# Kernel tuning notes

Measured on AMD Instinct MI355X. Metric: run time of the kernel, lower is better.

Reference implementation:

```python
import math
import jax, jax.numpy as jnp
import numpy as np


def conv2d(x, w, stride=1, padding=0, groups=1):
    return jax.lax.conv_general_dilated(
        x, w, (stride, stride), [(padding, padding), (padding, padding)],
        feature_group_count=groups, dimension_numbers=('NCHW', 'OIHW', 'NCHW'))


def bn_relu(x, g, b, eps=1e-5):
    # training-mode batchnorm (batch statistics, biased var) + ReLU
    m = x.mean(axis=(0, 2, 3), keepdims=True)
    v = x.var(axis=(0, 2, 3), keepdims=True)
    y = (x - m) * jax.lax.rsqrt(v + eps)
    return jax.nn.relu(y * g[None, :, None, None] + b[None, :, None, None])


def up2x(x):
    B, C, H, W = x.shape
    return jax.image.resize(x, (B, C, 2 * H, 2 * W), 'bilinear')


def pos2d(C, H, W):
    # faithful port of ReasonDecoder.pos2d -> [H*W, 1, C]
    dm = C // 2
    div = jnp.exp(jnp.arange(0.0, dm, 2.0) * (-(math.log(10000.0) / dm)))  # [dm//2]
    pos_w = jnp.arange(0.0, W)[:, None]
    pos_h = jnp.arange(0.0, H)[:, None]
    sw = jnp.sin(pos_w * div).T  # [dm//2, W]
    cw = jnp.cos(pos_w * div).T
    sh = jnp.sin(pos_h * div).T  # [dm//2, H]
    ch = jnp.cos(pos_h * div).T
    pe = jnp.zeros((C, H, W))
    pe = pe.at[0:dm:2].set(jnp.broadcast_to(sw[:, None, :], (dm // 2, H, W)))
    pe = pe.at[1:dm:2].set(jnp.broadcast_to(cw[:, None, :], (dm // 2, H, W)))
    pe = pe.at[dm::2].set(jnp.broadcast_to(sh[:, :, None], (dm // 2, H, W)))
    pe = pe.at[dm + 1::2].set(jnp.broadcast_to(ch[:, :, None], (dm // 2, H, W)))
    return pe.reshape(C, 1, H * W).transpose(2, 1, 0)


def setup_inputs() -> dict:
    key = jax.random.key(0)
    ks = jax.random.split(key, 32)
    B, C, H, W = 8, 512, 32, 32
    Cv = 256  # in_dim of Projector
    KS = 3
    s = 0.02
    inp = {
        'image_embeddings': jax.random.normal(ks[0], (B, C, H, W), jnp.float32),
        'sparse_prompt_embeddings': jax.random.normal(ks[1], (B, 2, C), jnp.float32),
        'state': jax.random.normal(ks[2], (B, C), jnp.float32),
        'multimask_output': 0,
        # stand-in transformer: single linear on (src + pos)
        'W_t': jax.random.normal(ks[3], (C, C), jnp.float32) * s,
        'iou_token': jax.random.normal(ks[4], (1, C), jnp.float32) * s,
        'mask_tokens': jax.random.normal(ks[5], (4, C), jnp.float32) * s,
        # Projector.vis
        'vis_conv1_w': jax.random.normal(ks[6], (2 * Cv, 2 * Cv, 3, 3), jnp.float32) * s,
        'vis_bn1_g': jnp.ones((2 * Cv,), jnp.float32),
        'vis_bn1_b': jnp.zeros((2 * Cv,), jnp.float32),
        'vis_conv2_w': jax.random.normal(ks[7], (Cv, 2 * Cv, 3, 3), jnp.float32) * s,
        'vis_bn2_g': jnp.ones((Cv,), jnp.float32),
        'vis_bn2_b': jnp.zeros((Cv,), jnp.float32),
        'vis_conv3_w': jax.random.normal(ks[8], (Cv, Cv, 1, 1), jnp.float32) * s,
        'vis_conv3_b': jnp.zeros((Cv,), jnp.float32),
        # Projector.txt -> Linear(512, 256*3*3 + 1)
        'txt_w': jax.random.normal(ks[9], (Cv * KS * KS + 1, C), jnp.float32) * s,
        'txt_b': jnp.zeros((Cv * KS * KS + 1,), jnp.float32),
        # 1x1 convs as linears
        'ln_ans_w': jax.random.normal(ks[10], (512, 512), jnp.float32) * s,
        'ln_ans_b': jnp.zeros((512,), jnp.float32),
        'ln_ans2_w': jax.random.normal(ks[11], (128, 512), jnp.float32) * s,
        'ln_ans2_b': jnp.zeros((128,), jnp.float32),
        # router: Linear(1024,256) -> ReLU -> Linear(256,8)
        'router_w1': jax.random.normal(ks[12], (256, 1024), jnp.float32) * s,
        'router_b1': jnp.zeros((256,), jnp.float32),
        'router_w2': jax.random.normal(ks[13], (8, 256), jnp.float32) * s,
        'router_b2': jnp.zeros((8,), jnp.float32),
        # 8 experts: Linear(128, 23) each, stacked
        'experts_w': jax.random.normal(ks[14], (8, 23, 128), jnp.float32) * s,
        'experts_b': jnp.zeros((8, 23), jnp.float32),
    }
    return inp


def reference(image_embeddings, sparse_prompt_embeddings, state, multimask_output,
              W_t, iou_token, mask_tokens,
              vis_conv1_w, vis_bn1_g, vis_bn1_b,
              vis_conv2_w, vis_bn2_g, vis_bn2_b,
              vis_conv3_w, vis_conv3_b,
              txt_w, txt_b, ln_ans_w, ln_ans_b, ln_ans2_w, ln_ans2_b,
              router_w1, router_b1, router_w2, router_b2,
              experts_w, experts_b):
    B, C, H, W = image_embeddings.shape
    pe = pos2d(C, H, W)  # [HW,1,C]

    # tokens = [iou, mask tokens, sparse prompts] (passed to transformer; hs unused)
    out_tok = jnp.concatenate([iou_token, mask_tokens], axis=0)  # [5,C]
    tokens = jnp.concatenate(
        [jnp.broadcast_to(out_tok[None], (B,) + out_tok.shape), sparse_prompt_embeddings], axis=1)
    del tokens  # hs is discarded by predict_masks

    # stand-in transformer: src_out = Linear(src_flat + pos)
    src_flat = image_embeddings.reshape(B, C, H * W).transpose(0, 2, 1) + pe[:, 0, :][None]  # [B,HW,C]
    src_flat = jnp.einsum('bnc,dc->bnd', src_flat, W_t)
    src = src_flat.transpose(0, 2, 1).reshape(B, C, H, W)

    # ---- Projector ----
    ans = src.mean(axis=(2, 3))                              # global avg pool [B,512]
    ans_vec = ans @ ln_ans_w.T + ln_ans_b                    # 1x1 conv [B,512]

    x = up2x(src)
    x = bn_relu(conv2d(x, vis_conv1_w, padding=1), vis_bn1_g, vis_bn1_b)
    x = up2x(x)
    x = bn_relu(conv2d(x, vis_conv2_w, padding=1), vis_bn2_g, vis_bn2_b)
    x = conv2d(x, vis_conv3_w) + vis_conv3_b[None, :, None, None]  # [B,256,4H,4W]
    Bx, Cx, Hx, Wx = x.shape

    qa = jnp.concatenate([state, ans_vec], axis=1)           # [B,1024]
    o = jax.nn.softmax(qa, axis=1) * qa
    half = o.shape[1] // 2
    word = o[:, :half] + o[:, half:]                         # [B,512]
    word = word @ txt_w.T + txt_b                            # [B, 256*9+1]
    dyn_w = word[:, :-1].reshape(B, Cx, 3, 3)                # per-sample conv weights
    dyn_b = word[:, -1]                                      # [B]

    xg = x.reshape(1, B * Cx, Hx, Wx)
    out = conv2d(xg, dyn_w, padding=1, groups=B) + dyn_b[None, :, None, None]  # [1,B,Hx,Wx]
    masks = out.transpose(1, 0, 2, 3)                        # [B,1,Hx,Wx]

    gates = jax.nn.softmax(
        jax.nn.relu(qa @ router_w1.T + router_b1) @ router_w2.T + router_b2, axis=1)  # [B,8]
    feat128 = ans_vec @ ln_ans2_w.T + ln_ans2_b              # [B,128]
    logits = jnp.einsum('be,eof,bf->bo', gates, experts_w, feat128) + gates @ experts_b  # [B,23]

    masks = masks[:, 1:, :, :] if multimask_output else masks[:, 0:1, :, :]
    return masks, logits, src
```

## Files before the change

### kernel.cpp

```cpp
#include <hip/hip_runtime.h>
#include <hip/hip_bf16.h>

typedef __attribute__((ext_vector_type(8))) short short8;
typedef __attribute__((ext_vector_type(4))) short shortx4;
typedef __attribute__((ext_vector_type(4))) float floatx4;
typedef __attribute__((ext_vector_type(16))) float floatx16;

#define F2BF __float2bfloat16
#define BF2F __bfloat162float

#define WS_W4R2   0UL
#define WS_WRO2   9437184UL
#define WS_WRO1   11796480UL
#define WS_Y1     16515072UL
#define WS_Y2     50069504UL
#define WS_W4R1   50069504UL
#define WS_A      68943872UL
#define WS_WTB    77332480UL
#define WS_SRCB   77856768UL
#define WS_STATS  117178368UL
#define WS_ANS    117186560UL
#define WS_QA     117207040UL
#define WS_ANSV   117239808UL
#define WS_WORD   117256192UL
#define WS_WORD2  117272576UL
#define WS_EFFW   117346336UL
#define WS_EFFB   117420064UL
#define WS_HID    117420352UL

#define OUT_LOGITS 131072
#define OUT_SRC    131256

__device__ __forceinline__ float inp(const void* p, long i, int isbf) {
    return isbf ? BF2F(((const __hip_bfloat16*)p)[i]) : ((const float*)p)[i];
}
__device__ __forceinline__ void outw(void* p, long i, float v, int isbf) {
    if (isbf) ((__hip_bfloat16*)p)[i] = F2BF(v);
    else      ((float*)p)[i] = v;
}
__device__ __forceinline__ float bfbits2f(short s) {
    unsigned int u = ((unsigned int)(unsigned short)s) << 16;
    float f; __builtin_memcpy(&f, &u, 4); return f;
}
__device__ __forceinline__ short f2bfbits(float f) {
    __hip_bfloat16 h = F2BF(f);
    short s; __builtin_memcpy(&s, &h, 2); return s;
}

__device__ __forceinline__ int detect_bf(const void* img) {
    const unsigned short* u = (const unsigned short*)img;
    int l = threadIdx.x & 63;
    int c = 0;
#pragma unroll
    for (int k = 0; k < 8; ++k) {
        int e = (u[(l * 8 + k) * 2] >> 7) & 0xFF;
        c += (e >= 100 && e <= 150) ? 1 : 0;
    }
    for (int off = 32; off; off >>= 1) c += __shfl_xor(c, off, 64);
    return c > 307;
}

__device__ __forceinline__ float pe_val(int n, int c) {
    float pos = (c < 256) ? (float)(n & 31) : (float)(n >> 5);
    int i = ((c < 256) ? c : (c - 256)) >> 1;
    float ang = pos * expf(-0.0719557841560639f * (float)i);
    return (c & 1) ? cosf(ang) : sinf(ang);
}

__global__ void k_pre(const void* __restrict__ img, const void* __restrict__ cw1,
                      const void* __restrict__ cw2, const void* __restrict__ Wt,
                      __hip_bfloat16* __restrict__ A,
                      __hip_bfloat16* __restrict__ W4R1, __hip_bfloat16* __restrict__ W4R2,
                      __hip_bfloat16* __restrict__ WRo1, __hip_bfloat16* __restrict__ WRo2,
                      __hip_bfloat16* __restrict__ WTB) {
    int isbf = detect_bf(img);
    int bid = blockIdx.x, tid = threadIdx.x;
    __shared__ float LS[2304];
    if (bid < 4096) {
        int nt = bid & 31, ct = (bid >> 5) & 15, b = bid >> 9;
        int tx = tid & 31, ty = tid >> 5;
        int c0 = ct * 32, n0 = nt * 32;
        for (int j = 0; j < 4; ++j) {
            int c = c0 + ty + j * 8;
            LS[(ty + j * 8) * 33 + tx] = inp(img, ((long)(b * 512 + c)) * 1024 + n0 + tx, isbf);
        }
        __syncthreads();
        for (int j = 0; j < 4; ++j) {
            int n = n0 + ty + j * 8, c = c0 + tx;
            A[((long)(b * 1024 + n)) * 512 + c] = F2BF(LS[tx * 33 + ty + j * 8] + pe_val(n, c));
        }
    } else if (bid < 5632) {
        int bb = bid - 4096;
        const void* w; __hip_bfloat16 *w4, *wo; int Cout, r0;
        if (bb < 1024) { w = cw1; w4 = W4R1; wo = WRo1; Cout = 512; r0 = bb * 256; }
        else           { w = cw2; w4 = W4R2; wo = WRo2; Cout = 256; r0 = (bb - 1024) * 256; }
        int Cout4 = Cout << 2;
        int co = r0 >> 9, ci0 = r0 & 511;
        for (int e = tid; e < 2304; e += 256) LS[e] = inp(w, (long)r0 * 9 + e, isbf);
        __syncthreads();
        int ci = ci0 + tid;
        int cc = ci >> 5, cw = ci & 31;
        float w9[9];
#pragma unroll
        for (int t = 0; t < 9; ++t) w9[t] = LS[tid * 9 + t];
#pragma unroll
        for (int t = 0; t < 9; ++t)
            wo[((long)(t * 16 + cc) * Cout + co) * 32 + cw] = F2BF(w9[t]);
        const float BY[2][3][3] = {{{0.75f, 0.25f, 0.f}, {0.25f, 0.75f, 0.75f}, {0.f, 0.f, 0.25f}},
                                   {{0.25f, 0.f, 0.f},  {0.75f, 0.75f, 0.25f}, {0.f, 0.25f, 0.75f}}};
#pragma unroll
        for (int p = 0; p < 4; ++p) {
            int py = p >> 1, px = p & 1;
#pragma unroll
            for (int dy = 0; dy < 3; ++dy)
#pragma unroll
            for (int dx = 0; dx < 3; ++dx) {
                float v = 0.f;
#pragma unroll
                for (int ky = 0; ky < 3; ++ky)
#pragma unroll
                for (int kx = 0; kx < 3; ++kx)
                    v += BY[py][dy][ky] * BY[px][dx][kx] * w9[ky * 3 + kx];
                w4[((long)((dy * 3 + dx) * 16 + cc) * Cout4 + p * Cout + co) * 32 + cw] = F2BF(v);
            }
        }
    } else {
        for (int i = (bid - 5632) * 256 + tid; i < 512 * 512; i += 256 * 256)
            WTB[i] = F2BF(inp(Wt, i, isbf));
    }
}

__global__ __launch_bounds__(256) void k_gemm1(const __hip_bfloat16* __restrict__ A,
                                               const __hip_bfloat16* __restrict__ Bw,
                                               __hip_bfloat16* __restrict__ srcB,
                                               void* __restrict__ dst,
                                               float* __restrict__ ANS,
                                               const void* __restrict__ img) {
    int isbf = detect_bf(img);
    __shared__ __align__(16) __hip_bfloat16 As[128 * 32];
    __shared__ __align__(16) __hip_bfloat16 Bs[128 * 32];
    int m0 = blockIdx.x * 128, n0 = blockIdx.y * 128;
    int tid = threadIdx.x;
    int wave = tid >> 6, l = tid & 63, lm = l & 15, q = l >> 4;
    int wm = wave & 1, wn = wave >> 1;
    int m_0 = tid >> 2, qq0 = tid & 3;
    int m_1 = (tid + 256) >> 2, qq1 = qq0;
    const __hip_bfloat16* aA0 = A + ((long)(m0 + m_0)) * 512 + qq0 * 8;
    const __hip_bfloat16* aB0 = Bw + ((long)(n0 + m_0)) * 512 + qq0 * 8;
    const __hip_bfloat16* aA1 = A + ((long)(m0 + m_1)) * 512 + qq1 * 8;
    const __hip_bfloat16* aB1 = Bw + ((long)(n0 + m_1)) * 512 + qq1 * 8;
    int wA0 = m_0 * 32 + qq0 * 8, wA1 = m_1 * 32 + qq1 * 8;
    short8 rA0 = *(const short8*)(aA0), rB0 = *(const short8*)(aB0);
    short8 rA1 = *(const short8*)(aA1), rB1 = *(const short8*)(aB1);
    floatx4 zero4 = {0.f, 0.f, 0.f, 0.f};
    floatx4 acc[4][4];
    for (int i = 0; i < 4; ++i) for (int j = 0; j < 4; ++j) acc[i][j] = zero4;
    for (int k0 = 0; k0 < 512; k0 += 32) {
        __syncthreads();
        *(short8*)(As + wA0) = rA0; *(short8*)(Bs + wA0) = rB0;
        *(short8*)(As + wA1) = rA1; *(short8*)(Bs + wA1) = rB1;
        __syncthreads();
        if (k0 < 480) {
            rA0 = *(const short8*)(aA0 + k0 + 32); rB0 = *(const short8*)(aB0 + k0 + 32);
            rA1 = *(const short8*)(aA1 + k0 + 32); rB1 = *(const short8*)(aB1 + k0 + 32);
        }
        short8 af[4], bfv[4];
#pragma unroll
        for (int t = 0; t < 4; ++t) af[t] = *(short8*)(As + (wm * 64 + t * 16 + lm) * 32 + q * 8);
#pragma unroll
        for (int t = 0; t < 4; ++t) bfv[t] = *(short8*)(Bs + (wn * 64 + t * 16 + lm) * 32 + q * 8);
#pragma unroll
        for (int i = 0; i < 4; ++i)
#pragma unroll
            for (int j = 0; j < 4; ++j)
                acc[i][j] = __builtin_amdgcn_mfma_f32_16x16x32_bf16(af[i], bfv[j], acc[i][j], 0, 0, 0);
    }
    int b = m0 >> 10, hw0 = m0 & 1023;
    float cs[4] = {0.f, 0.f, 0.f, 0.f};
#pragma unroll
    for (int i = 0; i < 4; ++i)
#pragma unroll
        for (int j = 0; j < 4; ++j) {
            int mrow = wm * 64 + i * 16 + q * 4;
            int n = n0 + wn * 64 + j * 16 + lm;
            long mg = (long)(m0 + mrow);
#pragma unroll
            for (int r = 0; r < 4; ++r) {
                float v = acc[i][j][r];
                srcB[(mg + r) * 512 + n] = F2BF(v);
                cs[j] += v;
            }
            long obase = (long)OUT_SRC + ((long)(b * 512 + n)) * 1024 + hw0 + mrow;
            if (isbf) {
                shortx4 pk = { f2bfbits(acc[i][j][0]), f2bfbits(acc[i][j][1]),
                               f2bfbits(acc[i][j][2]), f2bfbits(acc[i][j][3]) };
                *(shortx4*)((__hip_bfloat16*)dst + obase) = pk;
            } else {
                floatx4 pk = { acc[i][j][0], acc[i][j][1], acc[i][j][2], acc[i][j][3] };
                *(floatx4*)((float*)dst + obase) = pk;
            }
        }
#pragma unroll
    for (int j = 0; j < 4; ++j) {
        cs[j] += __shfl_xor(cs[j], 16);
        cs[j] += __shfl_xor(cs[j], 32);
    }
    __syncthreads();
    float* CS = (float*)Bs;
    if (wm == 1 && q == 0) {
#pragma unroll
        for (int j = 0; j < 4; ++j) CS[wn * 64 + j * 16 + lm] = cs[j];
    }
    __syncthreads();
    if (wm == 0 && q == 0) {
#pragma unroll
        for (int j = 0; j < 4; ++j) {
            int n = n0 + wn * 64 + j * 16 + lm;
            atomicAdd(ANS + b * 512 + n, cs[j] + CS[wn * 64 + j * 16 + lm]);
        }
    }
}

__global__ void k_ansvec(const float* __restrict__ ANS, const void* __restrict__ lw,
                         const void* __restrict__ lb, float* __restrict__ ansv,
                         const void* __restrict__ img) {
    int isbf = detect_bf(img);
    int b = blockIdx.x, dt = blockIdx.y, tid = threadIdx.x;
    __shared__ float aL[512];
    __shared__ float R[256];
    aL[tid] = ANS[b * 512 + tid] * (1.f / 1024.f);
    aL[tid + 256] = ANS[b * 512 + tid + 256] * (1.f / 1024.f);
    __syncthreads();
    int d = dt * 64 + (tid >> 2), cl = tid & 3;
    float acc = 0.f;
    for (int k = 0; k < 128; ++k) {
        int c = cl + 4 * k;
        acc += aL[c] * inp(lw, (long)d * 512 + c, isbf);
    }
    R[tid] = acc;
    __syncthreads();
    if (cl == 0)
        ansv[b * 512 + d] = R[tid] + R[tid + 1] + R[tid + 2] + R[tid + 3] + inp(lb, d, isbf);
}

__global__ void k_word(const float* __restrict__ ansv, const void* __restrict__ state,
                       float* __restrict__ qa, float* __restrict__ word,
                       const void* __restrict__ img) {
    int isbf = detect_bf(img);
    int b = blockIdx.x, tid = threadIdx.x;
    __shared__ float L[1024];
    __shared__ float red[256];
    L[tid] = inp(state, b * 512 + tid, isbf);
    L[tid + 256] = inp(state, b * 512 + tid + 256, isbf);
    L[tid + 512] = ansv[b * 512 + tid];
    L[tid + 768] = ansv[b * 512 + tid + 256];
    __syncthreads();
    for (int j = tid; j < 1024; j += 256) qa[b * 1024 + j] = L[j];
    float m = fmaxf(fmaxf(L[tid], L[tid + 256]), fmaxf(L[tid + 512], L[tid + 768]));
    red[tid] = m; __syncthreads();
    for (int s = 128; s > 0; s >>= 1) { if (tid < s) red[tid] = fmaxf(red[tid], red[tid + s]); __syncthreads(); }
    float M = red[0]; __syncthreads();
    float z = expf(L[tid] - M) + expf(L[tid + 256] - M) + expf(L[tid + 512] - M) + expf(L[tid + 768] - M);
    red[tid] = z; __syncthreads();
    for (int s = 128; s > 0; s >>= 1) { if (tid < s) red[tid] += red[tid + s]; __syncthreads(); }
    float Z = red[0];
    for (int j = tid; j < 512; j += 256) {
        float o1 = expf(L[j] - M) / Z * L[j];
        float o2 = expf(L[j + 512] - M) / Z * L[j + 512];
        word[b * 512 + j] = o1 + o2;
    }
}

__global__ void k_txt(const float* __restrict__ word, const void* __restrict__ tw,
                      const void* __restrict__ tb, float* __restrict__ word2,
                      const void* __restrict__ img) {
    int isbf = detect_bf(img);
    int n = blockIdx.x, tid = threadIdx.x;
    __shared__ float wL[8][512];
    __shared__ float red[256 * 8];
    for (int e = tid; e < 4096; e += 256) wL[e >> 9][e & 511] = word[e];
    __syncthreads();
    float acc[8] = {0, 0, 0, 0, 0, 0, 0, 0};
    for (int c = tid; c < 512; c += 256) {
        float tv = inp(tw, (long)n * 512 + c, isbf);
        for (int b = 0; b < 8; ++b) acc[b] += wL[b][c] * tv;
    }
    for (int b = 0; b < 8; ++b) red[tid * 8 + b] = acc[b];
    __syncthreads();
    for (int s = 128; s > 0; s >>= 1) {
        if (tid < s) for (int b = 0; b < 8; ++b) red[tid * 8 + b] += red[(tid + s) * 8 + b];
        __syncthreads();
    }
    if (tid < 8) word2[tid * 2305 + n] = red[tid] + inp(tb, n, isbf);
}

__global__ void k_eff(const float* __restrict__ word2, const void* __restrict__ w3,
                      const void* __restrict__ b3, float* __restrict__ effw,
                      float* __restrict__ effb, const void* __restrict__ img) {
    int isbf = detect_bf(img);
    int bid = blockIdx.x;
    int b = bid / 9, tap = bid - b * 9;
    int tid = threadIdx.x;
    __shared__ float dw[256];
    dw[tid] = word2[b * 2305 + tid * 9 + tap];
    __syncthreads();
    float acc = 0.f;
    for (int c = 0; c < 256; ++c) acc += dw[c] * inp(w3, c * 256 + tid, isbf);
    effw[(b * 9 + tap) * 256 + tid] = acc;
    if (tid == 0) {
        float e = 0.f;
        for (int c = 0; c < 256; ++c) e += dw[c] * inp(b3, c, isbf);
        effb[b * 9 + tap] = e;
    }
}

__device__ __forceinline__ void epi32(const floatx16& Acc, int pxbase, int co4,
        int csh, int Cout, int tY, int tX, int b, int OW2, int hi,
        __hip_bfloat16* __restrict__ out, float& s1, float& s2) {
    int par = co4 >> csh; int co = co4 & (Cout - 1);
    int fyo = par >> 1, fxo = par & 1;
#pragma unroll
    for (int r = 0; r < 16; ++r) {
        int row = (r & 3) + 8 * (r >> 2) + 4 * hi;
        int px = pxbase + row;
        int fy = (((tY << 3) + (px >> 4)) << 1) + fyo;
        int fx = (((tX << 4) + (px & 15)) << 1) + fxo;
        float v = Acc[r];
        out[(((long)(b * OW2 + fy)) * OW2 + fx) * Cout + co] = F2BF(v);
        s1 += v; s2 += v * v;
    }
}

__global__ __launch_bounds__(256, 3) void k_conv4(const __hip_bfloat16* __restrict__ in,
        const __hip_bfloat16* __restrict__ w4, __hip_bfloat16* __restrict__ out,
        int inH, int inW, int Cout, float* __restrict__ s1o, float* __restrict__ s2o,
        const float* __restrict__ bnS1, const float* __restrict__ bnS2,
        const void* __restrict__ g, const void* __restrict__ bb, float invN,
        const void* __restrict__ img) {
    int Cout4 = Cout << 2;
    int csh = (Cout == 512) ? 9 : 8;
    int tXn = inW >> 4, tYn = inH >> 3;
    int bid = blockIdx.y;
    int tX = bid % tXn; int tmp = bid / tXn; int tY = tmp % tYn; int b = tmp / tYn;
    int co0 = blockIdx.x * 128;
    __shared__ __align__(16) __hip_bfloat16 Hs[180 * 40];
    __shared__ float scT[512], shT[512];
    int tid = threadIdx.x;
    int l = tid & 63, l31 = l & 31, hi = l >> 5;
    int wave = tid >> 6;
    int wm = wave & 1, wn = wave >> 1;
    int dobn = (bnS1 != nullptr);
    if (dobn) {
        int isbf = detect_bf(img);
        for (int c = tid; c < 512; c += 256) {
            float m = bnS1[c] * invN, var = bnS2[c] * invN - m * m;
            float sc = inp(g, c, isbf) * rsqrtf(var + 1e-5f);
            scT[c] = sc; shT[c] = inp(bb, c, isbf) - m * sc;
        }
    }
    int R0 = (tY << 3) - 1, C0 = (tX << 4) - 1;
    long base = (long)b * inH * inW;
    int sub = tid & 3;
    const __hip_bfloat16* ga[3];
    int wo[3];
#pragma unroll
    for (int s = 0; s < 3; ++s) {
        int gi = tid + s * 256;
        int p = gi >> 2; if (p > 179) p = 179;
        int hy = p / 18, hx = p - hy * 18;
        int gr = R0 + hy; gr = gr < 0 ? 0 : (gr > inH - 1 ? inH - 1 : gr);
        int gc = C0 + hx; gc = gc < 0 ? 0 : (gc > inW - 1 ? inW - 1 : gc);
        ga[s] = in + (base + (long)gr * inW + gc) * 512 + sub * 8;
        wo[s] = p * 40 + sub * 8;
    }
    int has2 = (tid < 208);
    short8 r0 = *(const short8*)(ga[0]);
    short8 r1 = *(const short8*)(ga[1]);
    short8 r2 = {0, 0, 0, 0, 0, 0, 0, 0};
    if (has2) r2 = *(const short8*)(ga[2]);
    int hb0, hb1;
    {
        int px0 = wm * 64 + l31;
        int px1 = px0 + 32;
        hb0 = ((px0 >> 4) * 18 + (px0 & 15)) * 40 + hi * 8;
        hb1 = ((px1 >> 4) * 18 + (px1 & 15)) * 40 + hi * 8;
    }
    const __hip_bfloat16* wl = w4 + ((long)(co0 + wn * 64 + l31)) * 32 + hi * 8;
    long TS = (long)Cout4 * 512;
    long CS = (long)Cout4 * 32;
    short8 wS0[4], wS1[4], wS2[4];
#define LDW(S, t, c) { const __hip_bfloat16* _p = wl + (long)(t) * TS + (long)(c) * CS; \
    S[0] = *(const short8*)(_p);            S[1] = *(const short8*)(_p + 16); \
    S[2] = *(const short8*)(_p + 1024);     S[3] = *(const short8*)(_p + 1024 + 16); }
    floatx16 zero16 = {0,0,0,0,0,0,0,0,0,0,0,0,0,0,0,0};
    floatx16 a00 = zero16, a01 = zero16, a10 = zero16, a11 = zero16;
    LDW(wS0, 0, 0);
    for (int ci0 = 0; ci0 < 512; ci0 += 32) {
        int cc = ci0 >> 5;
        __syncthreads();
        if (dobn) {
            float scv[8], shv[8];
#pragma unroll
            for (int k = 0; k < 8; ++k) { int c = ci0 + sub * 8 + k; scv[k] = scT[c]; shv[k] = shT[c]; }
#pragma unroll
            for (int k = 0; k < 8; ++k) {
                float f0 = bfbits2f(r0[k]) * scv[k] + shv[k]; r0[k] = f2bfbits(f0 > 0.f ? f0 : 0.f);
                float f1 = bfbits2f(r1[k]) * scv[k] + shv[k]; r1[k] = f2bfbits(f1 > 0.f ? f1 : 0.f);
                float f2 = bfbits2f(r2[k]) * scv[k] + shv[k]; r2[k] = f2bfbits(f2 > 0.f ? f2 : 0.f);
            }
        }
        *(short8*)(Hs + wo[0]) = r0;
        *(short8*)(Hs + wo[1]) = r1;
        if (has2) *(short8*)(Hs + wo[2]) = r2;
        __syncthreads();
        if (ci0 < 480) {
            r0 = *(const short8*)(ga[0] + ci0 + 32);
            r1 = *(const short8*)(ga[1] + ci0 + 32);
            if (has2) r2 = *(const short8*)(ga[2] + ci0 + 32);
        }
#pragma unroll
        for (int tap = 0; tap < 9; ++tap) {
            {
                int nt = tap + 1, ncc = cc;
                if (nt == 9) { nt = 0; ncc = cc + 1; }
                if (ncc < 16) {
                    if (((tap + 1) % 3) == 0)      { LDW(wS0, nt, ncc); }
                    else if (((tap + 1) % 3) == 1) { LDW(wS1, nt, ncc); }
                    else                            { LDW(wS2, nt, ncc); }
                }
            }
            int dy = tap / 3, dx = tap - dy * 3;
            int ho = (dy * 18 + dx) * 40;
            short8 af00 = *(const short8*)(Hs + hb0 + ho);
            short8 af01 = *(const short8*)(Hs + hb0 + ho + 16);
            short8 af10 = *(const short8*)(Hs + hb1 + ho);
            short8 af11 = *(const short8*)(Hs + hb1 + ho + 16);
            if ((tap % 3) == 0) {
                a00 = __builtin_amdgcn_mfma_f32_32x32x16_bf16(af00, wS0[0], a00, 0, 0, 0);
                a00 = __builtin_amdgcn_mfma_f32_32x32x16_bf16(af01, wS0[1], a00, 0, 0, 0);
                a01 = __builtin_amdgcn_mfma_f32_32x32x16_bf16(af00, wS0[2], a01, 0, 0, 0);
                a01 = __builtin_amdgcn_mfma_f32_32x32x16_bf16(af01, wS0[3], a01, 0, 0, 0);
                a10 = __builtin_amdgcn_mfma_f32_32x32x16_bf16(af10, wS0[0], a10, 0, 0, 0);
                a10 = __builtin_amdgcn_mfma_f32_32x32x16_bf16(af11, wS0[1], a10, 0, 0, 0);
                a11 = __builtin_amdgcn_mfma_f32_32x32x16_bf16(af10, wS0[2], a11, 0, 0, 0);
                a11 = __builtin_amdgcn_mfma_f32_32x32x16_bf16(af11, wS0[3], a11, 0, 0, 0);
            } else if ((tap % 3) == 1) {
                a00 = __builtin_amdgcn_mfma_f32_32x32x16_bf16(af00, wS1[0], a00, 0, 0, 0);
                a00 = __builtin_amdgcn_mfma_f32_32x32x16_bf16(af01, wS1[1], a00, 0, 0, 0);
                a01 = __builtin_amdgcn_mfma_f32_32x32x16_bf16(af00, wS1[2], a01, 0, 0, 0);
                a01 = __builtin_amdgcn_mfma_f32_32x32x16_bf16(af01, wS1[3], a01, 0, 0, 0);
                a10 = __builtin_amdgcn_mfma_f32_32x32x16_bf16(af10, wS1[0], a10, 0, 0, 0);
                a10 = __builtin_amdgcn_mfma_f32_32x32x16_bf16(af11, wS1[1], a10, 0, 0, 0);
                a11 = __builtin_amdgcn_mfma_f32_32x32x16_bf16(af10, wS1[2], a11, 0, 0, 0);
                a11 = __builtin_amdgcn_mfma_f32_32x32x16_bf16(af11, wS1[3], a11, 0, 0, 0);
            } else {
                a00 = __builtin_amdgcn_mfma_f32_32x32x16_bf16(af00, wS2[0], a00, 0, 0, 0);
                a00 = __builtin_amdgcn_mfma_f32_32x32x16_bf16(af01, wS2[1], a00, 0, 0, 0);
                a01 = __builtin_amdgcn_mfma_f32_32x32x16_bf16(af00, wS2[2], a01, 0, 0, 0);
                a01 = __builtin_amdgcn_mfma_f32_32x32x16_bf16(af01, wS2[3], a01, 0, 0, 0);
                a10 = __builtin_amdgcn_mfma_f32_32x32x16_bf16(af10, wS2[0], a10, 0, 0, 0);
                a10 = __builtin_amdgcn_mfma_f32_32x32x16_bf16(af11, wS2[1], a10, 0, 0, 0);
                a11 = __builtin_amdgcn_mfma_f32_32x32x16_bf16(af10, wS2[2], a11, 0, 0, 0);
                a11 = __builtin_amdgcn_mfma_f32_32x32x16_bf16(af11, wS2[3], a11, 0, 0, 0);
            }
        }
    }
#undef LDW
    int OW2 = inW << 1;
    float s1v0 = 0.f, s2v0 = 0.f, s1v1 = 0.f, s2v1 = 0.f;
    {
        int pxb0 = wm * 64, pxb1 = wm * 64 + 32;
        int co4a = co0 + wn * 64 + l31;
        int co4b = co4a + 32;
        epi32(a00, pxb0, co4a, csh, Cout, tY, tX, b, OW2, hi, out, s1v0, s2v0);
        epi32(a10, pxb1, co4a, csh, Cout, tY, tX, b, OW2, hi, out, s1v0, s2v0);
        epi32(a01, pxb0, co4b, csh, Cout, tY, tX, b, OW2, hi, out, s1v1, s2v1);
        epi32(a11, pxb1, co4b, csh, Cout, tY, tX, b, OW2, hi, out, s1v1, s2v1);
    }
    s1v0 += __shfl_xor(s1v0, 32); s2v0 += __shfl_xor(s2v0, 32);
    s1v1 += __shfl_xor(s1v1, 32); s2v1 += __shfl_xor(s2v1, 32);
    __syncthreads();
    float* RB = (float*)Hs;
    if (wm == 1 && hi == 0) {
        int i0 = wn * 64 + l31, i1 = i0 + 32;
        RB[i0] = s1v0; RB[128 + i0] = s2v0;
        RB[i1] = s1v1; RB[128 + i1] = s2v1;
    }
    __syncthreads();
    if (wm == 0 && hi == 0) {
        int i0 = wn * 64 + l31, i1 = i0 + 32;
        atomicAdd(s1o + ((co0 + i0) & (Cout - 1)), s1v0 + RB[i0]);
        atomicAdd(s2o + ((co0 + i0) & (Cout - 1)), s2v0 + RB[128 + i0]);
        atomicAdd(s1o + ((co0 + i1) & (Cout - 1)), s1v1 + RB[i1]);
        atomicAdd(s2o + ((co0 + i1) & (Cout - 1)), s2v1 + RB[128 + i1]);
    }
}

__global__ __launch_bounds__(256) void k_efix(const __hip_bfloat16* __restrict__ in,
        __hip_bfloat16* __restrict__ Y, const __hip_bfloat16* __restrict__ wRo,
        int inW, int Cout, int ebase,
        float* __restrict__ s1o, float* __restrict__ s2o) {
    int OW = inW << 1;
    int coT = Cout >> 6;
    int b = blockIdx.x / coT, cot = blockIdx.x - b * coT;
    int co0 = cot << 6;
    int e = ebase + blockIdx.y;
    __shared__ __align__(16) __hip_bfloat16 E[130 * 40];
    __shared__ __align__(16) __hip_bfloat16 Lline[64 * 32];
    int tid = threadIdx.x;
    int wave = tid >> 6, l = tid & 63, lm = l & 15, q = l >> 4;
    int mspan = OW >> 2;
    int ilim = OW >> 6;
    int mb = wave * mspan;
    floatx4 zero4 = {0.f, 0.f, 0.f, 0.f};
    floatx4 acc[2][4];
    for (int i = 0; i < 2; ++i) for (int j = 0; j < 4; ++j) acc[i][j] = zero4;
    int lineG = inW * 4;
    int eG = (OW + 2) * 4;
    int haveL = (tid < lineG);
    const __hip_bfloat16* lbase = in;
    {
        int x = tid >> 2, sb = tid & 3;
        long gidx;
        if (e < 2) { int R = (e == 0) ? 0 : inW - 1; gidx = (long)(b * inW + R) * inW + x; }
        else       { int Cc = (e == 2) ? 0 : inW - 1; gidx = (long)(b * inW + x) * inW + Cc; }
        if (x >= inW) gidx = (long)b * inW * inW;
        lbase = in + gidx * 512 + sb * 8;
    }
    short8 rl = {0, 0, 0, 0, 0, 0, 0, 0};
    if (haveL) rl = *(const short8*)(lbase);
    for (int ci0 = 0; ci0 < 512; ci0 += 32) {
        __syncthreads();
        if (haveL) *(short8*)(Lline + tid * 8) = rl;
        __syncthreads();
        if (ci0 < 480 && haveL) rl = *(const short8*)(lbase + ci0 + 32);
        for (int t = tid; t < eG; t += 256) {
            int f1 = t >> 2, sb = t & 3;
            int f = f1 - 1;
            short8 res = {0, 0, 0, 0, 0, 0, 0, 0};
            if (f < 0 || f >= OW) {
                if (e < 2) { int xx = (f < 0) ? 0 : inW - 1; res = *(const short8*)(Lline + (xx * 4 + sb) * 8); }
            } else {
                int x0; float w0;
                if (f & 1) { x0 = f >> 1; w0 = 0.75f; } else { x0 = (f >> 1) - 1; w0 = 0.25f; }
                int x1 = x0 + 1;
                if (x0 < 0) x0 = 0;
                if (x1 > inW - 1) x1 = inW - 1;
                short8 v0 = *(const short8*)(Lline + (x0 * 4 + sb) * 8);
                short8 v1 = *(const short8*)(Lline + (x1 * 4 + sb) * 8);
                float w1c = 1.f - w0;
#pragma unroll
                for (int k = 0; k < 8; ++k)
                    res[k] = f2bfbits(w0 * bfbits2f(v0[k]) + w1c * bfbits2f(v1[k]));
            }
            *(short8*)(E + f1 * 40 + sb * 8) = res;
        }
        __syncthreads();
        int cc = ci0 >> 5;
#pragma unroll
        for (int t = 0; t < 3; ++t) {
            int tap = (e == 0) ? t : (e == 1) ? (6 + t) : (e == 2) ? (t * 3) : (t * 3 + 2);
            short8 bfv[4];
#pragma unroll
            for (int j = 0; j < 4; ++j)
                bfv[j] = *(const short8*)(wRo + ((long)(tap * 16 + cc) * Cout + co0 + j * 16 + lm) * 32 + q * 8);
#pragma unroll
            for (int i = 0; i < 2; ++i) {
                if (i < ilim) {
                    short8 af = *(const short8*)(E + (mb + i * 16 + lm + t) * 40 + q * 8);
#pragma unroll
                    for (int j = 0; j < 4; ++j)
                        acc[i][j] = __builtin_amdgcn_mfma_f32_16x16x32_bf16(af, bfv[j], acc[i][j], 0, 0, 0);
                }
            }
        }
    }
    float d1s[4] = {0.f, 0.f, 0.f, 0.f}, d2s[4] = {0.f, 0.f, 0.f, 0.f};
    for (int i = 0; i < ilim; ++i)
#pragma unroll
    for (int j = 0; j < 4; ++j) {
        int co = co0 + j * 16 + lm;
#pragma unroll
        for (int r = 0; r < 4; ++r) {
            int m = mb + i * 16 + q * 4 + r;
            int fy, fx;
            if (e == 0) { fy = 0; fx = m; }
            else if (e == 1) { fy = OW - 1; fx = m; }
            else if (e == 2) { fy = m; fx = 0; }
            else { fy = m; fx = OW - 1; }
            long a = (((long)(b * OW + fy)) * OW + fx) * Cout + co;
            float vo = BF2F(Y[a]);
            float vn = vo - acc[i][j][r];
            Y[a] = F2BF(vn);
            d1s[j] += vn - vo;
            d2s[j] += vn * vn - vo * vo;
        }
    }
#pragma unroll
    for (int j = 0; j < 4; ++j) {
        d1s[j] += __shfl_xor(d1s[j], 16); d1s[j] += __shfl_xor(d1s[j], 32);
        d2s[j] += __shfl_xor(d2s[j], 16); d2s[j] += __shfl_xor(d2s[j], 32);
    }
    if (q == 0) {
#pragma unroll
        for (int j = 0; j < 4; ++j) {
            atomicAdd(s1o + co0 + j * 16 + lm, d1s[j]);
            atomicAdd(s2o + co0 + j * 16 + lm, d2s[j]);
        }
    }
}

__global__ __launch_bounds__(256) void k_masks(const __hip_bfloat16* __restrict__ x2,
                                               const float* __restrict__ effw,
                                               const float* __restrict__ effb,
                                               const float* __restrict__ word2,
                                               void* __restrict__ mout,
                                               const float* __restrict__ s1,
                                               const float* __restrict__ s2,
                                               const void* __restrict__ g,
                                               const void* __restrict__ bb, float invN,
                                               const void* __restrict__ img) {
    int isbf = detect_bf(img);
    int bid = blockIdx.x;
    int tX = bid & 15, tY = (bid >> 4) & 15, b = bid >> 8;
    __shared__ __align__(16) __hip_bfloat16 H[100 * 264];
    __shared__ __align__(16) float EW[9 * 256];
    __shared__ float EB[9];
    __shared__ float sc2T[256];
    __shared__ float sh2T[256];
    int tid = threadIdx.x;
    {
        float m = s1[tid] * invN, var = s2[tid] * invN - m * m;
        float sc = inp(g, tid, isbf) * rsqrtf(var + 1e-5f);
        sc2T[tid] = sc; sh2T[tid] = inp(bb, tid, isbf) - m * sc;
    }
    __syncthreads();
    for (int e = tid; e < 3200; e += 256) {
        int c8 = e & 31, p = e >> 5;
        int hy = p / 10, hx = p - hy * 10;
        int gy = tY * 8 + hy - 1, gx = tX * 8 + hx - 1;
        short8 res = {0, 0, 0, 0, 0, 0, 0, 0};
        if (gy >= 0 && gy < 128 && gx >= 0 && gx < 128) {
            short8 raw = *(const short8*)(x2 + (((long)(b * 128 + gy)) * 128 + gx) * 256 + c8 * 8);
#pragma unroll
            for (int k = 0; k < 8; ++k) {
                int c = c8 * 8 + k;
                float v = bfbits2f(raw[k]) * sc2T[c] + sh2T[c];
                res[k] = f2bfbits(v > 0.f ? v : 0.f);
            }
        }
        *(short8*)(H + p * 264 + c8 * 8) = res;
    }
    for (int e = tid; e < 2304; e += 256) EW[e] = effw[b * 2304 + e];
    if (tid < 9) EB[tid] = effb[b * 9 + tid];
    __syncthreads();
    int px = tid & 63, part = tid >> 6;
    int py = px >> 3, pxc = px & 7;
    int cbase = part * 64;
    float acc = 0.f;
    for (int tap = 0; tap < 9; ++tap) {
        int ky = tap / 3, kx = tap - ky * 3;
        int hp = (py + ky) * 10 + pxc + kx;
        const __hip_bfloat16* hrow = H + (long)hp * 264 + cbase;
        const float* erow = EW + tap * 256 + cbase;
#pragma unroll
        for (int c8 = 0; c8 < 8; ++c8) {
            short8 h8 = *(const short8*)(hrow + c8 * 8);
            floatx4 e0 = *(const floatx4*)(erow + c8 * 8);
            floatx4 e1 = *(const floatx4*)(erow + c8 * 8 + 4);
            acc += bfbits2f(h8[0]) * e0[0] + bfbits2f(h8[1]) * e0[1] +
                   bfbits2f(h8[2]) * e0[2] + bfbits2f(h8[3]) * e0[3] +
                   bfbits2f(h8[4]) * e1[0] + bfbits2f(h8[5]) * e1[1] +
                   bfbits2f(h8[6]) * e1[2] + bfbits2f(h8[7]) * e1[3];
        }
    }
    float (*red)[64] = (float(*)[64])sc2T;
    red[part][px] = acc;
    __syncthreads();
    if (part == 0) {
        float s = red[0][px] + red[1][px] + red[2][px] + red[3][px];
        int oy = tY * 8 + py, ox = tX * 8 + pxc;
        float bias = word2[b * 2305 + 2304];
        for (int tap = 0; tap < 9; ++tap) {
            int ky = tap / 3, kx = tap - ky * 3;
            int iy = oy + ky - 1, ix = ox + kx - 1;
            if (iy >= 0 && iy < 128 && ix >= 0 && ix < 128) bias += EB[tap];
        }
        outw(mout, b * 16384 + oy * 128 + ox, s + bias, isbf);
    }
}

__global__ void k_hid(const float* __restrict__ qa, const void* __restrict__ w1,
                      const void* __restrict__ b1, float* __restrict__ hid,
                      const void* __restrict__ img) {
    int isbf = detect_bf(img);
    int b = blockIdx.x, ht = blockIdx.y, tid = threadIdx.x;
    __shared__ float qL[1024];
    __shared__ float R[256];
    for (int j = tid; j < 1024; j += 256) qL[j] = qa[b * 1024 + j];
    __syncthreads();
    int h = ht * 64 + (tid >> 2), cl = tid & 3;
    float acc = 0.f;
    for (int k = 0; k < 256; ++k) {
        int c = cl + 4 * k;
        acc += qL[c] * inp(w1, (long)h * 1024 + c, isbf);
    }
    R[tid] = acc;
    __syncthreads();
    if (cl == 0) {
        float v = R[tid] + R[tid + 1] + R[tid + 2] + R[tid + 3] + inp(b1, h, isbf);
        hid[b * 256 + h] = v > 0.f ? v : 0.f;
    }
}

__global__ void k_logits(const float* __restrict__ hid, const float* __restrict__ ansv,
                         const void* __restrict__ w2, const void* __restrict__ b2,
                         const void* __restrict__ lw2, const void* __restrict__ lb2,
                         const void* __restrict__ ew, const void* __restrict__ ebias,
                         void* __restrict__ out, const void* __restrict__ img) {
    int isbf = detect_bf(img);
    int b = blockIdx.x, tid = threadIdx.x;
    __shared__ float hidL[256], avL[512], gates[8], feat[128], R[256];
    hidL[tid] = hid[b * 256 + tid];
    for (int j = tid; j < 512; j += 256) avL[j] = ansv[b * 512 + j];
    __syncthreads();
    if (tid < 8) {
        float gl = inp(b2, tid, isbf);
        for (int j = 0; j < 256; ++j) gl += hidL[j] * inp(w2, tid * 256 + j, isbf);
        gates[tid] = gl;
    }
    int f = tid >> 1, half = tid & 1;
    float acc = 0.f;
    for (int k = 0; k < 256; ++k) {
        int c = half + 2 * k;
        acc += avL[c] * inp(lw2, (long)f * 512 + c, isbf);
    }
    R[tid] = acc;
    __syncthreads();
    if (tid == 0) {
        float mx = gates[0];
        for (int e = 1; e < 8; ++e) mx = fmaxf(mx, gates[e]);
        float z = 0.f;
        for (int e = 0; e < 8; ++e) { gates[e] = expf(gates[e] - mx); z += gates[e]; }
        for (int e = 0; e < 8; ++e) gates[e] /= z;
    }
    if (half == 0) feat[f] = R[tid] + R[tid + 1] + inp(lb2, f, isbf);
    __syncthreads();
    if (tid < 23) {
        float a = 0.f;
        for (int e = 0; e < 8; ++e) {
            float d = inp(ebias, e * 23 + tid, isbf);
            for (int ff = 0; ff < 128; ++ff) d += inp(ew, (e * 23 + tid) * 128 + ff, isbf) * feat[ff];
            a += gates[e] * d;
        }
        outw(out, OUT_LOGITS + b * 23 + tid, a, isbf);
    }
}

extern "C" void kernel_launch(void* const* d_in, const int* in_sizes, int n_in,
                              void* d_out, int out_size, void* d_ws, size_t ws_size,
                              hipStream_t stream) {
    (void)in_sizes; (void)n_in; (void)out_size; (void)ws_size;
    const void* img   = d_in[0];
    const void* state = d_in[2];
    const void* Wt    = d_in[4];
    const void* cw1   = d_in[7];
    const void* g1    = d_in[8];
    const void* bb1   = d_in[9];
    const void* cw2   = d_in[10];
    const void* g2    = d_in[11];
    const void* bb2   = d_in[12];
    const void* w3    = d_in[13];
    const void* b3    = d_in[14];
    const void* txtw  = d_in[15];
    const void* txtb  = d_in[16];
    const void* lnw   = d_in[17];
    const void* lnb   = d_in[18];
    const void* lnw2  = d_in[19];
    const void* lnb2  = d_in[20];
    const void* rw1   = d_in[21];
    const void* rb1   = d_in[22];
    const void* rw2   = d_in[23];
    const void* rb2   = d_in[24];
    const void* ew    = d_in[25];
    const void* eb    = d_in[26];

    char* ws = (char*)d_ws;
    __hip_bfloat16* W4R2 = (__hip_bfloat16*)(ws + WS_W4R2);
    __hip_bfloat16* WRO2 = (__hip_bfloat16*)(ws + WS_WRO2);
    __hip_bfloat16* WRO1 = (__hip_bfloat16*)(ws + WS_WRO1);
    __hip_bfloat16* Y1   = (__hip_bfloat16*)(ws + WS_Y1);
    __hip_bfloat16* Y2   = (__hip_bfloat16*)(ws + WS_Y2);
    __hip_bfloat16* W4R1 = (__hip_bfloat16*)(ws + WS_W4R1);
    __hip_bfloat16* A    = (__hip_bfloat16*)(ws + WS_A);
    __hip_bfloat16* WTB  = (__hip_bfloat16*)(ws + WS_WTB);
    __hip_bfloat16* SRCB = (__hip_bfloat16*)(ws + WS_SRCB);
    float* S1A = (float*)(ws + WS_STATS);
    float* S2A = S1A + 512;
    float* S1B = S1A + 1024;
    float* S2B = S1A + 1536;
    float* ANS   = (float*)(ws + WS_ANS);
    float* QA    = (float*)(ws + WS_QA);
    float* ANSV  = (float*)(ws + WS_ANSV);
    float* WORD  = (float*)(ws + WS_WORD);
    float* WORD2 = (float*)(ws + WS_WORD2);
    float* EFFW  = (float*)(ws + WS_EFFW);
    float* EFFB  = (float*)(ws + WS_EFFB);
    float* HID   = (float*)(ws + WS_HID);

    hipMemsetAsync(ws + WS_STATS, 0, 24576, stream);

    k_pre<<<5888, 256, 0, stream>>>(img, cw1, cw2, Wt, A, W4R1, W4R2, WRO1, WRO2, WTB);
    k_gemm1<<<dim3(64, 4), 256, 0, stream>>>(A, WTB, SRCB, d_out, ANS, img);
    k_ansvec<<<dim3(8, 8), 256, 0, stream>>>(ANS, lnw, lnb, ANSV, img);
    k_word<<<8, 256, 0, stream>>>(ANSV, state, QA, WORD, img);
    k_txt<<<2305, 256, 0, stream>>>(WORD, txtw, txtb, WORD2, img);
    k_eff<<<72, 256, 0, stream>>>(WORD2, w3, b3, EFFW, EFFB, img);
    k_conv4<<<dim3(16, 64), 256, 0, stream>>>(SRCB, W4R1, Y1, 32, 32, 512, S1A, S2A,
                                              nullptr, nullptr, nullptr, nullptr, 0.f, img);
    k_efix<<<dim3(64, 2), 256, 0, stream>>>(SRCB, Y1, WRO1, 32, 512, 0, S1A, S2A);
    k_efix<<<dim3(64, 2), 256, 0, stream>>>(SRCB, Y1, WRO1, 32, 512, 2, S1A, S2A);
    k_conv4<<<dim3(8, 256), 256, 0, stream>>>(Y1, W4R2, Y2, 64, 64, 256, S1B, S2B,
                                              S1A, S2A, g1, bb1, 1.f / 32768.f, img);
    k_efix<<<dim3(32, 2), 256, 0, stream>>>(Y1, Y2, WRO2, 64, 256, 0, S1B, S2B);
    k_efix<<<dim3(32, 2), 256, 0, stream>>>(Y1, Y2, WRO2, 64, 256, 2, S1B, S2B);
    k_masks<<<2048, 256, 0, stream>>>(Y2, EFFW, EFFB, WORD2, d_out,
                                      S1B, S2B, g2, bb2, 1.f / 131072.f, img);
    k_hid<<<dim3(8, 4), 256, 0, stream>>>(QA, rw1, rb1, HID, img);
    k_logits<<<8, 256, 0, stream>>>(HID, ANSV, rw2, rb2, lnw2, lnb2, ew, eb, d_out, img);
}
```

Before: 1.094 ms.

## Double-buffer conv4 halo tile in LDS with one barrier per channel chunk

```diff
diff --git a/kernel.cpp b/kernel.cpp
--- a/kernel.cpp
+++ b/kernel.cpp
@@ -343,21 +343,13 @@
     int bid = blockIdx.y;
     int tX = bid % tXn; int tmp = bid / tXn; int tY = tmp % tYn; int b = tmp / tYn;
     int co0 = blockIdx.x * 128;
-    __shared__ __align__(16) __hip_bfloat16 Hs[180 * 40];
+    __shared__ __align__(16) __hip_bfloat16 Hs[2][180 * 40];
     __shared__ float scT[512], shT[512];
     int tid = threadIdx.x;
     int l = tid & 63, l31 = l & 31, hi = l >> 5;
     int wave = tid >> 6;
     int wm = wave & 1, wn = wave >> 1;
     int dobn = (bnS1 != nullptr);
-    if (dobn) {
-        int isbf = detect_bf(img);
-        for (int c = tid; c < 512; c += 256) {
-            float m = bnS1[c] * invN, var = bnS2[c] * invN - m * m;
-            float sc = inp(g, c, isbf) * rsqrtf(var + 1e-5f);
-            scT[c] = sc; shT[c] = inp(bb, c, isbf) - m * sc;
-        }
-    }
     int R0 = (tY << 3) - 1, C0 = (tX << 4) - 1;
     long base = (long)b * inH * inW;
     int sub = tid & 3;
@@ -378,6 +370,31 @@
     short8 r1 = *(const short8*)(ga[1]);
     short8 r2 = {0, 0, 0, 0, 0, 0, 0, 0};
     if (has2) r2 = *(const short8*)(ga[2]);
+    if (dobn) {
+        int isbf = detect_bf(img);
+        for (int c = tid; c < 512; c += 256) {
+            float m = bnS1[c] * invN, var = bnS2[c] * invN - m * m;
+            float sc = inp(g, c, isbf) * rsqrtf(var + 1e-5f);
+            scT[c] = sc; shT[c] = inp(bb, c, isbf) - m * sc;
+        }
+    }
+    __syncthreads();
+    if (dobn) {
+        int cb = sub * 8;
+#pragma unroll
+        for (int k = 0; k < 8; ++k) {
+            float sc = scT[cb + k], sh = shT[cb + k];
+            float f0 = bfbits2f(r0[k]) * sc + sh; r0[k] = f2bfbits(f0 > 0.f ? f0 : 0.f);
+            float f1 = bfbits2f(r1[k]) * sc + sh; r1[k] = f2bfbits(f1 > 0.f ? f1 : 0.f);
+            float f2 = bfbits2f(r2[k]) * sc + sh; r2[k] = f2bfbits(f2 > 0.f ? f2 : 0.f);
+        }
+    }
+    *(short8*)(Hs[0] + wo[0]) = r0;
+    *(short8*)(Hs[0] + wo[1]) = r1;
+    if (has2) *(short8*)(Hs[0] + wo[2]) = r2;
+    r0 = *(const short8*)(ga[0] + 32);
+    r1 = *(const short8*)(ga[1] + 32);
+    if (has2) r2 = *(const short8*)(ga[2] + 32);
     int hb0, hb1;
     {
         int px0 = wm * 64 + l31;
@@ -395,34 +412,39 @@
     floatx16 zero16 = {0,0,0,0,0,0,0,0,0,0,0,0,0,0,0,0};
     floatx16 a00 = zero16, a01 = zero16, a10 = zero16, a11 = zero16;
     LDW(wS0, 0, 0);
-    for (int ci0 = 0; ci0 < 512; ci0 += 32) {
-        int cc = ci0 >> 5;
-        __syncthreads();
-        if (dobn) {
-            float scv[8], shv[8];
-#pragma unroll
-            for (int k = 0; k < 8; ++k) { int c = ci0 + sub * 8 + k; scv[k] = scT[c]; shv[k] = shT[c]; }
-#pragma unroll
-            for (int k = 0; k < 8; ++k) {
-                float f0 = bfbits2f(r0[k]) * scv[k] + shv[k]; r0[k] = f2bfbits(f0 > 0.f ? f0 : 0.f);
-                float f1 = bfbits2f(r1[k]) * scv[k] + shv[k]; r1[k] = f2bfbits(f1 > 0.f ? f1 : 0.f);
-                float f2 = bfbits2f(r2[k]) * scv[k] + shv[k]; r2[k] = f2bfbits(f2 > 0.f ? f2 : 0.f);
-            }
-        }
-        *(short8*)(Hs + wo[0]) = r0;
-        *(short8*)(Hs + wo[1]) = r1;
-        if (has2) *(short8*)(Hs + wo[2]) = r2;
-        __syncthreads();
-        if (ci0 < 480) {
-            r0 = *(const short8*)(ga[0] + ci0 + 32);
-            r1 = *(const short8*)(ga[1] + ci0 + 32);
-            if (has2) r2 = *(const short8*)(ga[2] + ci0 + 32);
-        }
+    asm volatile("s_waitcnt lgkmcnt(0)" ::: "memory");
+    __builtin_amdgcn_sched_barrier(0);
+    __builtin_amdgcn_s_barrier();
+    __builtin_amdgcn_sched_barrier(0);
+    for (int i = 0; i < 16; ++i) {
+        int rb = i & 1, wb = rb ^ 1;
+        if (i < 15) {
+            if (dobn) {
+                int cb = (i + 1) * 32 + sub * 8;
+#pragma unroll
+                for (int k = 0; k < 8; ++k) {
+                    float sc = scT[cb + k], sh = shT[cb + k];
+                    float f0 = bfbits2f(r0[k]) * sc + sh; r0[k] = f2bfbits(f0 > 0.f ? f0 : 0.f);
+                    float f1 = bfbits2f(r1[k]) * sc + sh; r1[k] = f2bfbits(f1 > 0.f ? f1 : 0.f);
+                    float f2 = bfbits2f(r2[k]) * sc + sh; r2[k] = f2bfbits(f2 > 0.f ? f2 : 0.f);
+                }
+            }
+            *(short8*)(Hs[wb] + wo[0]) = r0;
+            *(short8*)(Hs[wb] + wo[1]) = r1;
+            if (has2) *(short8*)(Hs[wb] + wo[2]) = r2;
+            if (i < 14) {
+                r0 = *(const short8*)(ga[0] + (i + 2) * 32);
+                r1 = *(const short8*)(ga[1] + (i + 2) * 32);
+                if (has2) r2 = *(const short8*)(ga[2] + (i + 2) * 32);
+            }
+        }
+        const __hip_bfloat16* HR = Hs[rb];
+        __builtin_amdgcn_s_setprio(1);
 #pragma unroll
         for (int tap = 0; tap < 9; ++tap) {
             {
-                int nt = tap + 1, ncc = cc;
-                if (nt == 9) { nt = 0; ncc = cc + 1; }
+                int nt = tap + 1, ncc = i;
+                if (nt == 9) { nt = 0; ncc = i + 1; }
                 if (ncc < 16) {
                     if (((tap + 1) % 3) == 0)      { LDW(wS0, nt, ncc); }
                     else if (((tap + 1) % 3) == 1) { LDW(wS1, nt, ncc); }
@@ -431,10 +453,10 @@
             }
             int dy = tap / 3, dx = tap - dy * 3;
             int ho = (dy * 18 + dx) * 40;
-            short8 af00 = *(const short8*)(Hs + hb0 + ho);
-            short8 af01 = *(const short8*)(Hs + hb0 + ho + 16);
-            short8 af10 = *(const short8*)(Hs + hb1 + ho);
-            short8 af11 = *(const short8*)(Hs + hb1 + ho + 16);
+            short8 af00 = *(const short8*)(HR + hb0 + ho);
+            short8 af01 = *(const short8*)(HR + hb0 + ho + 16);
+            short8 af10 = *(const short8*)(HR + hb1 + ho);
+            short8 af11 = *(const short8*)(HR + hb1 + ho + 16);
             if ((tap % 3) == 0) {
                 a00 = __builtin_amdgcn_mfma_f32_32x32x16_bf16(af00, wS0[0], a00, 0, 0, 0);
                 a00 = __builtin_amdgcn_mfma_f32_32x32x16_bf16(af01, wS0[1], a00, 0, 0, 0);
@@ -464,6 +486,11 @@
                 a11 = __builtin_amdgcn_mfma_f32_32x32x16_bf16(af11, wS2[3], a11, 0, 0, 0);
             }
         }
+        __builtin_amdgcn_s_setprio(0);
+        asm volatile("s_waitcnt lgkmcnt(0)" ::: "memory");
+        __builtin_amdgcn_sched_barrier(0);
+        __builtin_amdgcn_s_barrier();
+        __builtin_amdgcn_sched_barrier(0);
     }
 #undef LDW
     int OW2 = inW << 1;
```

Result: slower. 1.131 ms (+3.4%).

## Repack conv4 weights into fragment-contiguous layout and split LDS halo by subchunk

Applied to the files above, without the earlier changes.

```diff
diff --git a/kernel.cpp b/kernel.cpp
--- a/kernel.cpp
+++ b/kernel.cpp
@@ -95,11 +95,13 @@
         if (bb < 1024) { w = cw1; w4 = W4R1; wo = WRo1; Cout = 512; r0 = bb * 256; }
         else           { w = cw2; w4 = W4R2; wo = WRo2; Cout = 256; r0 = (bb - 1024) * 256; }
         int Cout4 = Cout << 2;
+        int G = Cout4 >> 5;
         int co = r0 >> 9, ci0 = r0 & 511;
         for (int e = tid; e < 2304; e += 256) LS[e] = inp(w, (long)r0 * 9 + e, isbf);
         __syncthreads();
         int ci = ci0 + tid;
         int cc = ci >> 5, cw = ci & 31;
+        int ksub = (ci >> 4) & 1, hic = (ci >> 3) & 1, ee = ci & 7;
         float w9[9];
 #pragma unroll
         for (int t = 0; t < 9; ++t) w9[t] = LS[tid * 9 + t];
@@ -111,6 +113,8 @@
 #pragma unroll
         for (int p = 0; p < 4; ++p) {
             int py = p >> 1, px = p & 1;
+            int co4 = p * Cout + co;
+            int cog = co4 >> 5, l31c = co4 & 31;
 #pragma unroll
             for (int dy = 0; dy < 3; ++dy)
 #pragma unroll
@@ -121,7 +125,9 @@
 #pragma unroll
                 for (int kx = 0; kx < 3; ++kx)
                     v += BY[py][dy][ky] * BY[px][dx][kx] * w9[ky * 3 + kx];
-                w4[((long)((dy * 3 + dx) * 16 + cc) * Cout4 + p * Cout + co) * 32 + cw] = F2BF(v);
+                long fi = ((((long)((dy * 3 + dx) * 16 + cc) * G + cog) * 2 + ksub) * 64
+                           + hic * 32 + l31c) * 8 + ee;
+                w4[fi] = F2BF(v);
             }
         }
     } else {
@@ -339,11 +345,12 @@
         const void* __restrict__ img) {
     int Cout4 = Cout << 2;
     int csh = (Cout == 512) ? 9 : 8;
+    int G = Cout4 >> 5;
     int tXn = inW >> 4, tYn = inH >> 3;
     int bid = blockIdx.y;
     int tX = bid % tXn; int tmp = bid / tXn; int tY = tmp % tYn; int b = tmp / tYn;
     int co0 = blockIdx.x * 128;
-    __shared__ __align__(16) __hip_bfloat16 Hs[180 * 40];
+    __shared__ __align__(16) __hip_bfloat16 Hs[4 * 180 * 8];
     __shared__ float scT[512], shT[512];
     int tid = threadIdx.x;
     int l = tid & 63, l31 = l & 31, hi = l >> 5;
@@ -371,27 +378,30 @@
         int gr = R0 + hy; gr = gr < 0 ? 0 : (gr > inH - 1 ? inH - 1 : gr);
         int gc = C0 + hx; gc = gc < 0 ? 0 : (gc > inW - 1 ? inW - 1 : gc);
         ga[s] = in + (base + (long)gr * inW + gc) * 512 + sub * 8;
-        wo[s] = p * 40 + sub * 8;
+        wo[s] = (sub * 180 + p) * 8;
     }
     int has2 = (tid < 208);
     short8 r0 = *(const short8*)(ga[0]);
     short8 r1 = *(const short8*)(ga[1]);
     short8 r2 = {0, 0, 0, 0, 0, 0, 0, 0};
     if (has2) r2 = *(const short8*)(ga[2]);
-    int hb0, hb1;
+    int qA = hi * 1440;
+    int qB = qA + 2880;
+    int h0, h1;
     {
         int px0 = wm * 64 + l31;
         int px1 = px0 + 32;
-        hb0 = ((px0 >> 4) * 18 + (px0 & 15)) * 40 + hi * 8;
-        hb1 = ((px1 >> 4) * 18 + (px1 & 15)) * 40 + hi * 8;
-    }
-    const __hip_bfloat16* wl = w4 + ((long)(co0 + wn * 64 + l31)) * 32 + hi * 8;
-    long TS = (long)Cout4 * 512;
-    long CS = (long)Cout4 * 32;
+        h0 = ((px0 >> 4) * 18 + (px0 & 15)) * 8;
+        h1 = ((px1 >> 4) * 18 + (px1 & 15)) * 8;
+    }
+    const __hip_bfloat16* wl2 = w4 + (long)l * 8;
+    int cg0 = (co0 >> 5) + wn * 2;
     short8 wS0[4], wS1[4], wS2[4];
-#define LDW(S, t, c) { const __hip_bfloat16* _p = wl + (long)(t) * TS + (long)(c) * CS; \
-    S[0] = *(const short8*)(_p);            S[1] = *(const short8*)(_p + 16); \
-    S[2] = *(const short8*)(_p + 1024);     S[3] = *(const short8*)(_p + 1024 + 16); }
+#define LDW(S, t, c) { long fb = (((long)((t) * 16 + (c)) * G + cg0) * 2) * 512; \
+    S[0] = *(const short8*)(wl2 + fb);             \
+    S[1] = *(const short8*)(wl2 + fb + 512);       \
+    S[2] = *(const short8*)(wl2 + fb + 1024);      \
+    S[3] = *(const short8*)(wl2 + fb + 1536); }
     floatx16 zero16 = {0,0,0,0,0,0,0,0,0,0,0,0,0,0,0,0};
     floatx16 a00 = zero16, a01 = zero16, a10 = zero16, a11 = zero16;
     LDW(wS0, 0, 0);
@@ -430,11 +440,11 @@
                 }
             }
             int dy = tap / 3, dx = tap - dy * 3;
-            int ho = (dy * 18 + dx) * 40;
-            short8 af00 = *(const short8*)(Hs + hb0 + ho);
-            short8 af01 = *(const short8*)(Hs + hb0 + ho + 16);
-            short8 af10 = *(const short8*)(Hs + hb1 + ho);
-            short8 af11 = *(const short8*)(Hs + hb1 + ho + 16);
+            int hoE = (dy * 18 + dx) * 8;
+            short8 af00 = *(const short8*)(Hs + qA + h0 + hoE);
+            short8 af01 = *(const short8*)(Hs + qB + h0 + hoE);
+            short8 af10 = *(const short8*)(Hs + qA + h1 + hoE);
+            short8 af11 = *(const short8*)(Hs + qB + h1 + hoE);
             if ((tap % 3) == 0) {
                 a00 = __builtin_amdgcn_mfma_f32_32x32x16_bf16(af00, wS0[0], a00, 0, 0, 0);
                 a00 = __builtin_amdgcn_mfma_f32_32x32x16_bf16(af01, wS0[1], a00, 0, 0, 0);
```

New measurement: 1.042 ms. -4.7%, faster.
